# Kernel tuning notes

Measured on AMD Instinct MI355X. Metric: run time of the kernel, lower is better.

Reference implementation:

```python
import jax, jax.numpy as jnp
import numpy as np

TOPK = 2  # matches init_kwargs topk


def setup_inputs() -> dict:
    key = jax.random.key(0)
    k1, k2 = jax.random.split(key)
    T, D, E = 32768, 4096, 16
    hidden_states = jax.random.normal(k1, (T, D), dtype=jnp.float32)
    wg_weight = jax.random.normal(k2, (E, D), dtype=jnp.float32) * 0.02  # [num_experts, hidden]
    return {"hidden_states": hidden_states, "wg_weight": wg_weight}


def reference(hidden_states, wg_weight):
    # logits = hidden_states @ wg.T  -> [T, E], computed in fp32 as in the torch module
    logits = jnp.einsum("td,ed->te", hidden_states.astype(jnp.float32), wg_weight.astype(jnp.float32))
    gates = jax.nn.softmax(logits, axis=-1)  # [T, E]
    topk_weights, topk_indices = jax.lax.top_k(gates, TOPK)  # [T, K] each
    topk_weights = topk_weights / jnp.sum(topk_weights, axis=-1, keepdims=True)
    return topk_indices, topk_weights.astype(hidden_states.dtype)
```

## Files before the change

kernel.cpp:

```cpp
#include <hip/hip_runtime.h>
#include <math.h>

#define T_TOKENS 32768
#define HID      4096
#define NEXP     16
#define MT       8
#define WAVES    4
#define D4       (HID / 4)
#define KI       (D4 / 64)

typedef float f32x4 __attribute__((ext_vector_type(4)));

__global__ __launch_bounds__(256, 2) void moe_gate_kernel(
    const float* __restrict__ h,
    const float* __restrict__ w,
    float* __restrict__ out)
{
    __shared__ f32x4 sw[2][NEXP][64];

    const int lane = threadIdx.x & 63;
    const int wv   = threadIdx.x >> 6;
    const int t0   = (blockIdx.x * WAVES + wv) * MT;

    const f32x4* __restrict__ w4 = reinterpret_cast<const f32x4*>(w);
    const f32x4* hrow[MT];
    #pragma unroll
    for (int t = 0; t < MT; ++t)
        hrow[t] = reinterpret_cast<const f32x4*>(h + (size_t)(t0 + t) * HID);

    float acc[MT * NEXP];
    #pragma unroll
    for (int i = 0; i < MT * NEXP; ++i) acc[i] = 0.0f;

#define STAGE(b, ki_) do {                                                    \
        _Pragma("unroll")                                                     \
        for (int j = 0; j < 4; ++j) {                                         \
            const int e_ = wv * 4 + j;                                        \
            const f32x4* gsrc = w4 + (size_t)e_ * D4 + (ki_) * 64 + lane;     \
            __builtin_amdgcn_global_load_lds(                                 \
                (const __attribute__((address_space(1))) void*)gsrc,          \
                (__attribute__((address_space(3))) void*)&sw[b][e_][0],       \
                16, 0, 0);                                                    \
        }                                                                     \
    } while (0)

#define LOADH(dst, ki_) do {                                                  \
        const int d4_ = (ki_) * 64 + lane;                                    \
        _Pragma("unroll")                                                     \
        for (int t = 0; t < MT; ++t)                                          \
            dst[t] = __builtin_nontemporal_load(&hrow[t][d4_]);               \
    } while (0)

#define COMPUTE(b, hreg) do {                                                 \
        _Pragma("unroll")                                                     \
        for (int e_ = 0; e_ < NEXP; ++e_) {                                   \
            f32x4 wvv = sw[b][e_][lane];                                      \
            _Pragma("unroll")                                                 \
            for (int t = 0; t < MT; ++t) {                                    \
                float a = acc[t * NEXP + e_];                                 \
                a = fmaf(hreg[t][0], wvv[0], a);                              \
                a = fmaf(hreg[t][1], wvv[1], a);                              \
                a = fmaf(hreg[t][2], wvv[2], a);                              \
                a = fmaf(hreg[t][3], wvv[3], a);                              \
                acc[t * NEXP + e_] = a;                                       \
            }                                                                 \
        }                                                                     \
    } while (0)

    f32x4 hv[MT];
    STAGE(0, 0);
    LOADH(hv, 0);
    asm volatile("s_waitcnt vmcnt(8)" ::: "memory");
    __builtin_amdgcn_s_barrier();
    asm volatile("" ::: "memory");
    __builtin_amdgcn_sched_barrier(0);

    int cur = 0;
    for (int ki = 0; ki < KI - 1; ++ki) {
        STAGE(cur ^ 1, ki + 1);
        f32x4 hn[MT];
        LOADH(hn, ki + 1);
        COMPUTE(cur, hv);
        #pragma unroll
        for (int t = 0; t < MT; ++t) hv[t] = hn[t];
        asm volatile("s_waitcnt vmcnt(8)" ::: "memory");
        __builtin_amdgcn_s_barrier();
        asm volatile("" ::: "memory");
        __builtin_amdgcn_sched_barrier(0);
        cur ^= 1;
    }
    COMPUTE(cur, hv);

#define BUTTERFLY(base) do {                                                  \
        _Pragma("unroll")                                                     \
        for (int b = 32; b >= 1; b >>= 1) {                                   \
            const bool hi_ = (lane & b) != 0;                                 \
            _Pragma("unroll")                                                 \
            for (int j = 0; j < b; ++j) {                                     \
                float lo_v = acc[(base) + j];                                 \
                float hi_v = acc[(base) + j + b];                             \
                float keepv = hi_ ? hi_v : lo_v;                              \
                float sendv = hi_ ? lo_v : hi_v;                              \
                acc[(base) + j] = keepv + __shfl_xor(sendv, b, 64);           \
            }                                                                 \
        }                                                                     \
    } while (0)

    BUTTERFLY(0);
    BUTTERFLY(64);
    const float logit0 = acc[0];
    const float logit1 = acc[64];

    const int eidx = lane & 15;
#define TOP2_WRITE(logit_, tok_) do {                                         \
        float m1 = (logit_); int i1 = eidx;                                   \
        _Pragma("unroll")                                                     \
        for (int s = 1; s < 16; s <<= 1) {                                    \
            float ov = __shfl_xor(m1, s, 64);                                 \
            int   oi = __shfl_xor(i1, s, 64);                                 \
            if (ov > m1 || (ov == m1 && oi < i1)) { m1 = ov; i1 = oi; }       \
        }                                                                     \
        float masked = (eidx == i1) ? -INFINITY : (logit_);                   \
        float m2 = masked; int i2 = eidx;                                     \
        _Pragma("unroll")                                                     \
        for (int s = 1; s < 16; s <<= 1) {                                    \
            float ov = __shfl_xor(m2, s, 64);                                 \
            int   oi = __shfl_xor(i2, s, 64);                                 \
            if (ov > m2 || (ov == m2 && oi < i2)) { m2 = ov; i2 = oi; }       \
        }                                                                     \
        if (eidx == 0) {                                                      \
            const float r_ = expf(m2 - m1);                                   \
            const float s_ = 1.0f / (1.0f + r_);                              \
            float2* oidx = reinterpret_cast<float2*>(out);                    \
            float2* owt  = reinterpret_cast<float2*>(out + 2 * T_TOKENS);     \
            oidx[tok_] = make_float2((float)i1, (float)i2);                   \
            owt[tok_]  = make_float2(s_, r_ * s_);                            \
        }                                                                     \
    } while (0)

    TOP2_WRITE(logit0, t0 + (lane >> 4));
    TOP2_WRITE(logit1, t0 + 4 + (lane >> 4));

#undef STAGE
#undef LOADH
#undef COMPUTE
#undef BUTTERFLY
#undef TOP2_WRITE
}

extern "C" void kernel_launch(void* const* d_in, const int* in_sizes, int n_in,
                              void* d_out, int out_size, void* d_ws, size_t ws_size,
                              hipStream_t stream) {
    const float* h = (const float*)d_in[0];
    const float* w = (const float*)d_in[1];
    float* out = (float*)d_out;

    const int blocks = T_TOKENS / (MT * WAVES);
    moe_gate_kernel<<<blocks, 256, 0, stream>>>(h, w, out);
}
```

Measured before the change: 117.9 us.

## Stage half of gate weights in LDS per block, removing per-chunk barriers

Doubles the block to 512 threads (8 waves) and stages half the gate weight matrix (16 experts x 2048 floats, 128 KB) into LDS in one go, twice per block. The per-chunk barrier and double-buffered weight pipeline are replaced by a barrier-free inner loop that only prefetches hidden-state chunks. This cuts synchronisation overhead, but the large LDS footprint limits occupancy, and the weight load at each half is a full stall with no overlap.

```diff
diff --git a/kernel.cpp b/kernel.cpp
--- a/kernel.cpp
+++ b/kernel.cpp
@@ -5,22 +5,23 @@
 #define HID      4096
 #define NEXP     16
 #define MT       8
-#define WAVES    4
+#define WAVES    8
 #define D4       (HID / 4)
-#define KI       (D4 / 64)
+#define HALF     (D4 / 2)
+#define NC       (HALF / 64)
 
 typedef float f32x4 __attribute__((ext_vector_type(4)));
 
-__global__ __launch_bounds__(256, 2) void moe_gate_kernel(
+__global__ __launch_bounds__(512, 2) void moe_gate_kernel(
     const float* __restrict__ h,
     const float* __restrict__ w,
     float* __restrict__ out)
 {
-    __shared__ f32x4 sw[2][NEXP][64];
+    __shared__ f32x4 sw[NEXP][HALF];
 
     const int lane = threadIdx.x & 63;
     const int wv   = threadIdx.x >> 6;
-    const int t0   = (blockIdx.x * WAVES + wv) * MT;
+    const int t0   = blockIdx.x * (MT * WAVES) + wv * MT;
 
     const f32x4* __restrict__ w4 = reinterpret_cast<const f32x4*>(w);
     const f32x4* hrow[MT];
@@ -32,29 +33,31 @@
     #pragma unroll
     for (int i = 0; i < MT * NEXP; ++i) acc[i] = 0.0f;
 
-#define STAGE(b, ki_) do {                                                    \
+#define STAGE(kh_) do {                                                       \
         _Pragma("unroll")                                                     \
-        for (int j = 0; j < 4; ++j) {                                         \
-            const int e_ = wv * 4 + j;                                        \
-            const f32x4* gsrc = w4 + (size_t)e_ * D4 + (ki_) * 64 + lane;     \
+        for (int j = 0; j < 16; ++j) {                                        \
+            const int e_ = 2 * wv + (j >> 3);                                 \
+            const int c_ = j & 7;                                             \
+            const f32x4* gsrc =                                               \
+                w4 + (size_t)e_ * D4 + (kh_) * HALF + c_ * 64 + lane;         \
             __builtin_amdgcn_global_load_lds(                                 \
                 (const __attribute__((address_space(1))) void*)gsrc,          \
-                (__attribute__((address_space(3))) void*)&sw[b][e_][0],       \
+                (__attribute__((address_space(3))) void*)&sw[e_][c_ * 64],    \
                 16, 0, 0);                                                    \
         }                                                                     \
     } while (0)
 
-#define LOADH(dst, ki_) do {                                                  \
-        const int d4_ = (ki_) * 64 + lane;                                    \
+#define LOADH(dst, kh_, c_) do {                                              \
+        const int d4_ = (kh_) * HALF + (c_) * 64 + lane;                      \
         _Pragma("unroll")                                                     \
         for (int t = 0; t < MT; ++t)                                          \
             dst[t] = __builtin_nontemporal_load(&hrow[t][d4_]);               \
     } while (0)
 
-#define COMPUTE(b, hreg) do {                                                 \
+#define COMPUTE(c_, hreg) do {                                                \
         _Pragma("unroll")                                                     \
         for (int e_ = 0; e_ < NEXP; ++e_) {                                   \
-            f32x4 wvv = sw[b][e_][lane];                                      \
+            f32x4 wvv = sw[e_][(c_) * 64 + lane];                             \
             _Pragma("unroll")                                                 \
             for (int t = 0; t < MT; ++t) {                                    \
                 float a = acc[t * NEXP + e_];                                 \
@@ -67,29 +70,31 @@
         }                                                                     \
     } while (0)
 
-    f32x4 hv[MT];
-    STAGE(0, 0);
-    LOADH(hv, 0);
-    asm volatile("s_waitcnt vmcnt(8)" ::: "memory");
-    __builtin_amdgcn_s_barrier();
-    asm volatile("" ::: "memory");
-    __builtin_amdgcn_sched_barrier(0);
+    f32x4 hv[MT], hn[MT];
 
-    int cur = 0;
-    for (int ki = 0; ki < KI - 1; ++ki) {
-        STAGE(cur ^ 1, ki + 1);
-        f32x4 hn[MT];
-        LOADH(hn, ki + 1);
-        COMPUTE(cur, hv);
-        #pragma unroll
-        for (int t = 0; t < MT; ++t) hv[t] = hn[t];
+    for (int kh = 0; kh < 2; ++kh) {
+        if (kh) {
+            asm volatile("s_waitcnt lgkmcnt(0)" ::: "memory");
+            __builtin_amdgcn_s_barrier();
+            asm volatile("" ::: "memory");
+        }
+        STAGE(kh);
+        __builtin_amdgcn_sched_barrier(0);
+        LOADH(hv, kh, 0);
         asm volatile("s_waitcnt vmcnt(8)" ::: "memory");
         __builtin_amdgcn_s_barrier();
         asm volatile("" ::: "memory");
         __builtin_amdgcn_sched_barrier(0);
-        cur ^= 1;
+
+        #pragma unroll 1
+        for (int c = 0; c < NC - 1; ++c) {
+            LOADH(hn, kh, c + 1);
+            COMPUTE(c, hv);
+            #pragma unroll
+            for (int t = 0; t < MT; ++t) hv[t] = hn[t];
+        }
+        COMPUTE(NC - 1, hv);
     }
-    COMPUTE(cur, hv);
 
 #define BUTTERFLY(base) do {                                                  \
         _Pragma("unroll")                                                     \
@@ -156,5 +161,5 @@
     float* out = (float*)d_out;
 
     const int blocks = T_TOKENS / (MT * WAVES);
-    moe_gate_kernel<<<blocks, 256, 0, stream>>>(h, w, out);
+    moe_gate_kernel<<<blocks, 512, 0, stream>>>(h, w, out);
 }
```

Result: faster. 112.9 us (-4.3%).
